# Kernel tuning notes

Measured on AMD Instinct MI355X. Metric: run time of the kernel, lower is better.

The kernel has to match this reference:

```python
import jax, jax.numpy as jnp
import numpy as np

EMBED_DIM = 1024
NUM_HEADS = 16
B, L = 4, 2048


def setup_inputs() -> dict:
    key = jax.random.key(0)
    ks = jax.random.split(key, 5)
    scale = 0.02
    return {
        "x": jax.random.normal(ks[0], (B, L, EMBED_DIM), dtype=jnp.float32),
        "Wqkv_w": jax.random.normal(ks[1], (3 * EMBED_DIM, EMBED_DIM), dtype=jnp.float32) * scale,
        "Wqkv_b": jax.random.normal(ks[2], (3 * EMBED_DIM,), dtype=jnp.float32) * scale,
        "out_w": jax.random.normal(ks[3], (EMBED_DIM, EMBED_DIM), dtype=jnp.float32) * scale,
        "out_b": jax.random.normal(ks[4], (EMBED_DIM,), dtype=jnp.float32) * scale,
    }


def reference(x, Wqkv_w, Wqkv_b, out_w, out_b):
    Bb, Ll, D = x.shape
    H = NUM_HEADS
    hd = D // H
    # fused QKV projection (torch Linear: x @ W.T + b)
    qkv = jnp.einsum("bld,ed->ble", x, Wqkv_w) + Wqkv_b  # [B, L, 3D]
    q, k, v = jnp.split(qkv, 3, axis=-1)
    # [B, H, L, hd]
    q = q.reshape(Bb, Ll, H, hd).transpose(0, 2, 1, 3)
    k = k.reshape(Bb, Ll, H, hd).transpose(0, 2, 1, 3)
    v = v.reshape(Bb, Ll, H, hd).transpose(0, 2, 1, 3)
    scale = 1.0 / jnp.sqrt(jnp.asarray(hd, dtype=x.dtype))
    scores = jnp.einsum("bhqd,bhkd->bhqk", q, k) * scale  # [B, H, L, L]
    # causal mask (upper triangle above diagonal masked)
    causal = jnp.tril(jnp.ones((Ll, Ll), dtype=bool))
    scores = jnp.where(causal, scores, jnp.asarray(-jnp.inf, dtype=scores.dtype))
    attn = jax.nn.softmax(scores, axis=-1)
    attn_out = jnp.einsum("bhqk,bhkd->bhqd", attn, v)  # [B, H, L, hd]
    attn_out = attn_out.transpose(0, 2, 1, 3).reshape(Bb, Ll, D)
    out = jnp.einsum("bld,ed->ble", attn_out, out_w) + out_b
    return out
```

## Files before the change

### kernel.cpp

```cpp
#include <hip/hip_runtime.h>
#include <stdint.h>

#define DEV __device__ __forceinline__

typedef unsigned short u16;
typedef __bf16 bf16x8 __attribute__((ext_vector_type(8)));
typedef float f32x4 __attribute__((ext_vector_type(4)));
typedef u16 u16x8 __attribute__((ext_vector_type(8)));

#define MFMA_BF16(A, B, C) __builtin_amdgcn_mfma_f32_16x16x32_bf16(A, B, C, 0, 0, 0)
#define EXP2(x) __builtin_amdgcn_exp2f(x)

DEV u16 f2bf(float f) {
    unsigned x;
    __builtin_memcpy(&x, &f, 4);
    unsigned r = (x + 0x7fffu + ((x >> 16) & 1u)) >> 16;
    return (u16)r;
}

DEV u16 f2bf_fast(float f) {
    unsigned x;
    __builtin_memcpy(&x, &f, 4);
    return (u16)((x + 0x8000u) >> 16);
}

DEV void storeC(u16* p, float v) { *p = f2bf(v); }
DEV void storeC(float* p, float v) { *p = v; }

DEV void async_copy16(const u16* g, u16* l) {
    __builtin_amdgcn_global_load_lds(
        (__attribute__((address_space(1))) unsigned int*)g,
        (__attribute__((address_space(3))) unsigned int*)l, 16, 0, 0);
}

constexpr int N_X = 8192 * 1024, N_WQ = 3072 * 1024, N_WO = 1024 * 1024;

__global__ __launch_bounds__(256)
void cvt_all(const float* __restrict__ x, const float* __restrict__ wq,
             const float* __restrict__ wo, u16* __restrict__ out) {
    const int i = (blockIdx.x * 256 + threadIdx.x) * 4;
    const float* src;
    if (i < N_X) src = x + i;
    else if (i < N_X + N_WQ) src = wq + (i - N_X);
    else src = wo + (i - N_X - N_WQ);
    const float4 v = *(const float4*)src;
    ushort4 o;
    o.x = f2bf(v.x);
    o.y = f2bf(v.y);
    o.z = f2bf(v.z);
    o.w = f2bf(v.w);
    *(ushort4*)(out + i) = o;
}

template <typename OT, bool VSPLIT>
__global__ __launch_bounds__(256, 2)
void gemm_bt_bias(const u16* __restrict__ A, const u16* __restrict__ Bw,
                  const float* __restrict__ bias, OT* __restrict__ C,
                  u16* __restrict__ vT, int M, int N, int K) {
    __shared__ __attribute__((aligned(16))) u16 sA[2][128 * 32];
    __shared__ __attribute__((aligned(16))) u16 sB[2][128 * 32];

    const int tid  = threadIdx.x;
    const int lane = tid & 63;
    const int wave = tid >> 6;
    const int m0 = blockIdx.x * 128;
    const int n0 = blockIdx.y * 128;
    const int wm = (wave & 1) * 64;
    const int wn = (wave >> 1) * 64;
    const int fr = lane & 15;
    const int q4 = lane >> 4;

    const int r0 = tid >> 2;
    const int c0 = (tid & 3) * 8;
    const u16* gA0 = A + (size_t)(m0 + r0) * K + c0;
    const u16* gA1 = A + (size_t)(m0 + 64 + r0) * K + c0;
    const u16* gB0 = Bw + (size_t)(n0 + r0) * K + c0;
    const u16* gB1 = Bw + (size_t)(n0 + 64 + r0) * K + c0;

    f32x4 acc[4][4];
#pragma unroll
    for (int i = 0; i < 4; i++)
#pragma unroll
        for (int j = 0; j < 4; j++) acc[i][j] = (f32x4){0.f, 0.f, 0.f, 0.f};

    for (int k0 = 0; k0 < K; k0 += 64) {
#pragma unroll
        for (int p = 0; p < 2; ++p) {
            async_copy16(gA0 + k0 + p * 32, &sA[p][tid * 8]);
            async_copy16(gA1 + k0 + p * 32, &sA[p][2048 + tid * 8]);
            async_copy16(gB0 + k0 + p * 32, &sB[p][tid * 8]);
            async_copy16(gB1 + k0 + p * 32, &sB[p][2048 + tid * 8]);
        }
        __syncthreads();

#pragma unroll
        for (int p = 0; p < 2; ++p) {
            bf16x8 af[4], bfr[4];
#pragma unroll
            for (int i = 0; i < 4; i++)
                af[i] = *(const bf16x8*)&sA[p][(wm + i * 16 + fr) * 32 + q4 * 8];
#pragma unroll
            for (int j = 0; j < 4; j++)
                bfr[j] = *(const bf16x8*)&sB[p][(wn + j * 16 + fr) * 32 + q4 * 8];
#pragma unroll
            for (int i = 0; i < 4; i++)
#pragma unroll
                for (int j = 0; j < 4; j++)
                    acc[i][j] = MFMA_BF16(af[i], bfr[j], acc[i][j]);
        }
        __syncthreads();
    }

#pragma unroll
    for (int j = 0; j < 4; j++) {
        const int col = n0 + wn + j * 16 + fr;
        const float bv = bias[col];
        if (VSPLIT && col >= 2048) {
#pragma unroll
            for (int i = 0; i < 4; i++) {
                const int row = m0 + wm + i * 16 + q4 * 4;
                ushort4 o;
                o.x = f2bf(acc[i][j][0] + bv);
                o.y = f2bf(acc[i][j][1] + bv);
                o.z = f2bf(acc[i][j][2] + bv);
                o.w = f2bf(acc[i][j][3] + bv);
                *(ushort4*)&vT[(size_t)(col - 2048) * 8192 + row] = o;
            }
        } else {
#pragma unroll
            for (int i = 0; i < 4; i++) {
                const int row = m0 + wm + i * 16 + q4 * 4;
#pragma unroll
                for (int r = 0; r < 4; r++)
                    storeC(&C[(size_t)(row + r) * N + col], acc[i][j][r] + bv);
            }
        }
    }
}

constexpr int Lc = 2048, Dc = 1024;

__global__ __launch_bounds__(256, 2)
void attn_fa(const u16* __restrict__ qkv, const u16* __restrict__ vT,
             u16* __restrict__ outb) {
    __shared__ __attribute__((aligned(16))) u16 sK[2][64 * 64];
    __shared__ __attribute__((aligned(16))) u16 sVT[2][64 * 64];
    __shared__ __attribute__((aligned(16))) u16 sP[4][4][16 * 72];

    const int tid  = threadIdx.x;
    const int lane = tid & 63;
    const int wave = tid >> 6;
    const int fr = lane & 15;
    const int q4 = lane >> 4;
    const int f7 = fr & 7;

    const int id = blockIdx.x;
    const int g  = (id & 7) + 8 * (id >> 6);
    const int bx = (id >> 3) & 7;
    const int h = g & 15;
    const int b = g >> 4;
    const int qA = bx, qB = 15 - bx, qC = 16 + bx, qD = 31 - bx;

    constexpr float CEXP = 0.18033688011112042f;
    constexpr float MOFF = 16.0f * CEXP;

    bf16x8 qfA[2], qfB[2], qfC[2], qfD[2];
#define LOADQ(qf, qblk)                                                     \
    {                                                                       \
        const int qrow = (qblk) * 64 + wave * 16 + fr;                      \
        const u16* qp = qkv + ((size_t)(b * Lc + qrow) * 3) * Dc + h * 64;  \
        qf[0] = *(const bf16x8*)(qp + q4 * 8);                              \
        qf[1] = *(const bf16x8*)(qp + 32 + q4 * 8);                         \
    }
    LOADQ(qfA, qA) LOADQ(qfB, qB) LOADQ(qfC, qC) LOADQ(qfD, qD)
#undef LOADQ

    f32x4 oA[4], oB[4], oC[4], oD[4];
#pragma unroll
    for (int t = 0; t < 4; t++) {
        oA[t] = (f32x4){0.f, 0.f, 0.f, 0.f};
        oB[t] = (f32x4){0.f, 0.f, 0.f, 0.f};
        oC[t] = (f32x4){0.f, 0.f, 0.f, 0.f};
        oD[t] = (f32x4){0.f, 0.f, 0.f, 0.f};
    }
    float lA = 0.f, lB = 0.f, lC = 0.f, lD = 0.f;

    const int q_local = wave * 16 + fr;

    const int rr = tid >> 3;
    const int oo = tid & 7;
    const int wchk = (oo ^ (rr & 7)) * 8;
    const u16* kg = qkv + ((size_t)(b * Lc) * 3 + 1) * Dc + h * 64 + oo * 8;
    const u16* vg = vT + (size_t)(h * 64) * 8192 + b * Lc + oo * 8;

    u16x8 kr[2], vr[2];
#define LOADT(jb1)                                                                \
    _Pragma("unroll") for (int c = 0; c < 2; ++c) {                               \
        kr[c] = *(const u16x8*)(kg + (size_t)((jb1) * 64 + c * 32 + rr) * 3072);  \
        vr[c] = *(const u16x8*)(vg + (size_t)(c * 32 + rr) * 8192 + (jb1) * 64);  \
    }
#define WRT(bufi)                                                                 \
    _Pragma("unroll") for (int c = 0; c < 2; ++c) {                               \
        *(u16x8*)&sK[bufi][(c * 32 + rr) * 64 + wchk] = kr[c];                    \
        *(u16x8*)&sVT[bufi][(c * 32 + rr) * 64 + wchk] = vr[c];                   \
    }

    u16* sPA = &sP[wave][0][0];
    u16* sPB = &sP[wave][1][0];
    u16* sPC = &sP[wave][2][0];
    u16* sPD = &sP[wave][3][0];

#define SM_TILE(S, lS, sPp, qblk)                                           \
    {                                                                       \
        if (jb == (qblk)) {                                                 \
            _Pragma("unroll") for (int t = 0; t < 4; t++)                   \
                _Pragma("unroll") for (int r = 0; r < 4; r++)               \
                    if (t * 16 + q4 * 4 + r > q_local) S[t][r] = -1e30f;    \
        }                                                                   \
        _Pragma("unroll") for (int t = 0; t < 4; t++) {                     \
            _Pragma("unroll") for (int r = 0; r < 4; r++) {                 \
                const float p = EXP2(__builtin_fmaf(S[t][r], CEXP, -MOFF)); \
                S[t][r] = p;                                                \
                lS += p;                                                    \
            }                                                               \
            ushort4 o;                                                      \
            o.x = f2bf_fast(S[t][0]);                                       \
            o.y = f2bf_fast(S[t][1]);                                       \
            o.z = f2bf_fast(S[t][2]);                                       \
            o.w = f2bf_fast(S[t][3]);                                       \
            *(ushort4*)&sPp[fr * 72 + t * 16 + q4 * 4] = o;                 \
        }                                                                   \
    }

    LOADT(0);
    WRT(0);
    LOADT(1);
    __syncthreads();

    for (int jb = 0; jb <= qD; ++jb) {
        const u16* cK = sK[jb & 1];
        const u16* cV = sVT[jb & 1];

        if (jb < qD) WRT((jb & 1) ^ 1);
        if (jb + 2 <= qD) LOADT(jb + 2);

        const bool doA = (jb <= qA);
        const bool doB = (jb <= qB);
        const bool doC = (jb <= qC);

        f32x4 sA_[4], sB_[4], sC_[4], sD_[4];
#pragma unroll
        for (int t = 0; t < 4; t++) {
            const int row = (t * 16 + fr) * 64;
            const bf16x8 kf0 = *(const bf16x8*)&cK[row + (q4 ^ f7) * 8];
            const bf16x8 kf1 = *(const bf16x8*)&cK[row + ((4 + q4) ^ f7) * 8];
            sD_[t] = (f32x4){0.f, 0.f, 0.f, 0.f};
            sD_[t] = MFMA_BF16(kf0, qfD[0], sD_[t]);
            sD_[t] = MFMA_BF16(kf1, qfD[1], sD_[t]);
            if (doC) {
                sC_[t] = (f32x4){0.f, 0.f, 0.f, 0.f};
                sC_[t] = MFMA_BF16(kf0, qfC[0], sC_[t]);
                sC_[t] = MFMA_BF16(kf1, qfC[1], sC_[t]);
            }
            if (doB) {
                sB_[t] = (f32x4){0.f, 0.f, 0.f, 0.f};
                sB_[t] = MFMA_BF16(kf0, qfB[0], sB_[t]);
                sB_[t] = MFMA_BF16(kf1, qfB[1], sB_[t]);
            }
            if (doA) {
                sA_[t] = (f32x4){0.f, 0.f, 0.f, 0.f};
                sA_[t] = MFMA_BF16(kf0, qfA[0], sA_[t]);
                sA_[t] = MFMA_BF16(kf1, qfA[1], sA_[t]);
            }
        }

        SM_TILE(sD_, lD, sPD, qD);
        if (doC) SM_TILE(sC_, lC, sPC, qC);
        if (doB) SM_TILE(sB_, lB, sPB, qB);
        if (doA) SM_TILE(sA_, lA, sPA, qA);

#pragma unroll
        for (int ks = 0; ks < 2; ++ks) {
            const bf16x8 pfD = *(const bf16x8*)&sPD[fr * 72 + ks * 32 + q4 * 8];
            bf16x8 pfC, pfB, pfA;
            if (doC) pfC = *(const bf16x8*)&sPC[fr * 72 + ks * 32 + q4 * 8];
            if (doB) pfB = *(const bf16x8*)&sPB[fr * 72 + ks * 32 + q4 * 8];
            if (doA) pfA = *(const bf16x8*)&sPA[fr * 72 + ks * 32 + q4 * 8];
#pragma unroll
            for (int t = 0; t < 4; t++) {
                const bf16x8 vf =
                    *(const bf16x8*)&cV[(t * 16 + fr) * 64 + ((ks * 4 + q4) ^ f7) * 8];
                oD[t] = MFMA_BF16(vf, pfD, oD[t]);
                if (doC) oC[t] = MFMA_BF16(vf, pfC, oC[t]);
                if (doB) oB[t] = MFMA_BF16(vf, pfB, oB[t]);
                if (doA) oA[t] = MFMA_BF16(vf, pfA, oA[t]);
            }
        }
        __syncthreads();
    }
#undef SM_TILE
#undef LOADT
#undef WRT

#define WR_OUT(oS, lS, qblk)                                                      \
    {                                                                             \
        float lt = lS;                                                            \
        lt += __shfl_xor(lt, 16);                                                 \
        lt += __shfl_xor(lt, 32);                                                 \
        const float rl = 1.0f / lt;                                               \
        u16* orow =                                                               \
            outb + (size_t)(b * Lc + (qblk) * 64 + wave * 16 + fr) * Dc + h * 64; \
        _Pragma("unroll") for (int t = 0; t < 4; t++) {                           \
            ushort4 o;                                                            \
            o.x = f2bf(oS[t][0] * rl);                                            \
            o.y = f2bf(oS[t][1] * rl);                                            \
            o.z = f2bf(oS[t][2] * rl);                                            \
            o.w = f2bf(oS[t][3] * rl);                                            \
            *(ushort4*)(orow + t * 16 + q4 * 4) = o;                              \
        }                                                                         \
    }
    WR_OUT(oA, lA, qA)
    WR_OUT(oB, lB, qB)
    WR_OUT(oC, lC, qC)
    WR_OUT(oD, lD, qD)
#undef WR_OUT
}

extern "C" void kernel_launch(void* const* d_in, const int* in_sizes, int n_in,
                              void* d_out, int out_size, void* d_ws, size_t ws_size,
                              hipStream_t stream) {
    const float* x    = (const float*)d_in[0];
    const float* wqkv = (const float*)d_in[1];
    const float* bqkv = (const float*)d_in[2];
    const float* wout = (const float*)d_in[3];
    const float* bout = (const float*)d_in[4];
    float* out = (float*)d_out;

    u16* qkv    = (u16*)d_ws;
    u16* attn   = qkv + (size_t)8192 * 3072;
    u16* xbf    = attn + (size_t)8192 * 1024;
    u16* wqkvbf = xbf + (size_t)8192 * 1024;
    u16* woutbf = wqkvbf + (size_t)3072 * 1024;
    u16* vT     = woutbf + (size_t)1024 * 1024;

    dim3 blk(256);
    cvt_all<<<(N_X + N_WQ + N_WO) / 1024, blk, 0, stream>>>(x, wqkv, wout, xbf);

    gemm_bt_bias<u16, true><<<dim3(8192 / 128, 3072 / 128), blk, 0, stream>>>(
        xbf, wqkvbf, bqkv, qkv, vT, 8192, 3072, 1024);
    attn_fa<<<dim3(512), blk, 0, stream>>>(qkv, vT, attn);
    gemm_bt_bias<float, false><<<dim3(8192 / 128, 1024 / 128), blk, 0, stream>>>(
        attn, woutbf, bout, out, nullptr, 8192, 1024, 1024);
}
```

Before: 252.0 us.

## Keep softmax probabilities in registers, remapping V fragment loads to match

Drops the per-wave shared-memory staging buffer for the P tile. The S accumulator layout from the QK^T MFMA is packed straight into the B operand for the PV MFMA, and the V^T shared-memory reads are reordered into two 4-element halves so the k-index permutation matches. This removes the LDS write/read round trip and frees shared memory. In exchange it adds twice as many narrower LDS loads for V plus register shuffles, and it needs more live registers.

```diff
diff --git a/kernel.cpp b/kernel.cpp
--- a/kernel.cpp
+++ b/kernel.cpp
@@ -5,6 +5,7 @@
 
 typedef unsigned short u16;
 typedef __bf16 bf16x8 __attribute__((ext_vector_type(8)));
+typedef __bf16 bf16x4 __attribute__((ext_vector_type(4)));
 typedef float f32x4 __attribute__((ext_vector_type(4)));
 typedef u16 u16x8 __attribute__((ext_vector_type(8)));
 
@@ -145,7 +146,6 @@
              u16* __restrict__ outb) {
     __shared__ __attribute__((aligned(16))) u16 sK[2][64 * 64];
     __shared__ __attribute__((aligned(16))) u16 sVT[2][64 * 64];
-    __shared__ __attribute__((aligned(16))) u16 sP[4][4][16 * 72];
 
     const int tid  = threadIdx.x;
     const int lane = tid & 63;
@@ -205,30 +205,32 @@
         *(u16x8*)&sVT[bufi][(c * 32 + rr) * 64 + wchk] = vr[c];                   \
     }
 
-    u16* sPA = &sP[wave][0][0];
-    u16* sPB = &sP[wave][1][0];
-    u16* sPC = &sP[wave][2][0];
-    u16* sPD = &sP[wave][3][0];
-
-#define SM_TILE(S, lS, sPp, qblk)                                           \
+#define DO_TILE(qf, lS, pf, qblk)                                           \
     {                                                                       \
+        f32x4 S[4];                                                         \
+        _Pragma("unroll") for (int t = 0; t < 4; t++) {                     \
+            S[t] = (f32x4){0.f, 0.f, 0.f, 0.f};                             \
+            S[t] = MFMA_BF16(kf[t][0], qf[0], S[t]);                        \
+            S[t] = MFMA_BF16(kf[t][1], qf[1], S[t]);                        \
+        }                                                                   \
         if (jb == (qblk)) {                                                 \
             _Pragma("unroll") for (int t = 0; t < 4; t++)                   \
                 _Pragma("unroll") for (int r = 0; r < 4; r++)               \
                     if (t * 16 + q4 * 4 + r > q_local) S[t][r] = -1e30f;    \
         }                                                                   \
-        _Pragma("unroll") for (int t = 0; t < 4; t++) {                     \
+        _Pragma("unroll") for (int t = 0; t < 4; t++)                       \
             _Pragma("unroll") for (int r = 0; r < 4; r++) {                 \
                 const float p = EXP2(__builtin_fmaf(S[t][r], CEXP, -MOFF)); \
                 S[t][r] = p;                                                \
                 lS += p;                                                    \
             }                                                               \
-            ushort4 o;                                                      \
-            o.x = f2bf_fast(S[t][0]);                                       \
-            o.y = f2bf_fast(S[t][1]);                                       \
-            o.z = f2bf_fast(S[t][2]);                                       \
-            o.w = f2bf_fast(S[t][3]);                                       \
-            *(ushort4*)&sPp[fr * 72 + t * 16 + q4 * 4] = o;                 \
+        _Pragma("unroll") for (int ks = 0; ks < 2; ++ks) {                  \
+            u16x8 w;                                                        \
+            _Pragma("unroll") for (int j = 0; j < 4; j++) {                 \
+                w[j] = f2bf_fast(S[2 * ks][j]);                             \
+                w[4 + j] = f2bf_fast(S[2 * ks + 1][j]);                     \
+            }                                                               \
+            __builtin_memcpy(&pf[ks], &w, 16);                              \
         }                                                                   \
     }
 
@@ -248,57 +250,40 @@
         const bool doB = (jb <= qB);
         const bool doC = (jb <= qC);
 
-        f32x4 sA_[4], sB_[4], sC_[4], sD_[4];
+        bf16x8 kf[4][2];
 #pragma unroll
         for (int t = 0; t < 4; t++) {
             const int row = (t * 16 + fr) * 64;
-            const bf16x8 kf0 = *(const bf16x8*)&cK[row + (q4 ^ f7) * 8];
-            const bf16x8 kf1 = *(const bf16x8*)&cK[row + ((4 + q4) ^ f7) * 8];
-            sD_[t] = (f32x4){0.f, 0.f, 0.f, 0.f};
-            sD_[t] = MFMA_BF16(kf0, qfD[0], sD_[t]);
-            sD_[t] = MFMA_BF16(kf1, qfD[1], sD_[t]);
-            if (doC) {
-                sC_[t] = (f32x4){0.f, 0.f, 0.f, 0.f};
-                sC_[t] = MFMA_BF16(kf0, qfC[0], sC_[t]);
-                sC_[t] = MFMA_BF16(kf1, qfC[1], sC_[t]);
+            kf[t][0] = *(const bf16x8*)&cK[row + (q4 ^ f7) * 8];
+            kf[t][1] = *(const bf16x8*)&cK[row + ((4 + q4) ^ f7) * 8];
+        }
+
+        bf16x8 pfA[2], pfB[2], pfC[2], pfD[2];
+        DO_TILE(qfD, lD, pfD, qD);
+        if (doC) DO_TILE(qfC, lC, pfC, qC);
+        if (doB) DO_TILE(qfB, lB, pfB, qB);
+        if (doA) DO_TILE(qfA, lA, pfA, qA);
+
+#pragma unroll
+        for (int ks = 0; ks < 2; ++ks) {
+#pragma unroll
+            for (int t = 0; t < 4; t++) {
+                const int rowb = (t * 16 + fr) * 64;
+                const int sub = (q4 & 1) * 4;
+                const bf16x4 vlo = *(const bf16x4*)
+                    &cV[rowb + (((4 * ks + (q4 >> 1))) ^ f7) * 8 + sub];
+                const bf16x4 vhi = *(const bf16x4*)
+                    &cV[rowb + (((4 * ks + 2 + (q4 >> 1))) ^ f7) * 8 + sub];
+                const bf16x8 vf = __builtin_shufflevector(vlo, vhi, 0, 1, 2, 3, 4, 5, 6, 7);
+                oD[t] = MFMA_BF16(vf, pfD[ks], oD[t]);
+                if (doC) oC[t] = MFMA_BF16(vf, pfC[ks], oC[t]);
+                if (doB) oB[t] = MFMA_BF16(vf, pfB[ks], oB[t]);
+                if (doA) oA[t] = MFMA_BF16(vf, pfA[ks], oA[t]);
             }
-            if (doB) {
-                sB_[t] = (f32x4){0.f, 0.f, 0.f, 0.f};
-                sB_[t] = MFMA_BF16(kf0, qfB[0], sB_[t]);
-                sB_[t] = MFMA_BF16(kf1, qfB[1], sB_[t]);
-            }
-            if (doA) {
-                sA_[t] = (f32x4){0.f, 0.f, 0.f, 0.f};
-                sA_[t] = MFMA_BF16(kf0, qfA[0], sA_[t]);
-                sA_[t] = MFMA_BF16(kf1, qfA[1], sA_[t]);
-            }
-        }
-
-        SM_TILE(sD_, lD, sPD, qD);
-        if (doC) SM_TILE(sC_, lC, sPC, qC);
-        if (doB) SM_TILE(sB_, lB, sPB, qB);
-        if (doA) SM_TILE(sA_, lA, sPA, qA);
-
-#pragma unroll
-        for (int ks = 0; ks < 2; ++ks) {
-            const bf16x8 pfD = *(const bf16x8*)&sPD[fr * 72 + ks * 32 + q4 * 8];
-            bf16x8 pfC, pfB, pfA;
-            if (doC) pfC = *(const bf16x8*)&sPC[fr * 72 + ks * 32 + q4 * 8];
-            if (doB) pfB = *(const bf16x8*)&sPB[fr * 72 + ks * 32 + q4 * 8];
-            if (doA) pfA = *(const bf16x8*)&sPA[fr * 72 + ks * 32 + q4 * 8];
-#pragma unroll
-            for (int t = 0; t < 4; t++) {
-                const bf16x8 vf =
-                    *(const bf16x8*)&cV[(t * 16 + fr) * 64 + ((ks * 4 + q4) ^ f7) * 8];
-                oD[t] = MFMA_BF16(vf, pfD, oD[t]);
-                if (doC) oC[t] = MFMA_BF16(vf, pfC, oC[t]);
-                if (doB) oB[t] = MFMA_BF16(vf, pfB, oB[t]);
-                if (doA) oA[t] = MFMA_BF16(vf, pfA, oA[t]);
-            }
         }
         __syncthreads();
     }
-#undef SM_TILE
+#undef DO_TILE
 #undef LOADT
 #undef WRT
 
```

Result: faster. 241.9 us (-4.0%).
